# Kernel optimization log

Measured on AMD Instinct MI355X. Metric: run time of the kernel, lower is better.

The kernel has to match this reference:

```python
import jax, jax.numpy as jnp
import numpy as np

EPS = 1e-07
ROUTINGS = 3


def squash(s):
    # s: [..., d]
    n2 = jnp.sum(s * s, axis=-1, keepdims=True)
    return s * (n2 / (1.0 + n2) / jnp.sqrt(n2 + EPS))


def setup_inputs() -> dict:
    key = jax.random.key(0)
    k1, k2 = jax.random.split(key)
    B, I, P = 32, 2048, 16   # batch, input capsules, input capsule dim
    J, D = 32, 32            # output capsules, output capsule dim
    inputs = jax.random.normal(k1, (B, I, P), dtype=jnp.float32)
    # glorot-ish scale so squash operates in a reasonable range
    W = jax.random.normal(k2, (1, I, J, P, D), dtype=jnp.float32) * 0.05
    return {"inputs": inputs, "W": W}


def reference(inputs, W):
    # inputs: [B, I, P]; W: [1, I, J, P, D]
    Wm = W[0]  # [I, J, P, D]
    # u_hat[b,i,j,d] = sum_p W[i,j,p,d] * inputs[b,i,p]
    u_hat = jnp.einsum('bip,ijpd->bijd', inputs, Wm)  # [B, I, J, D]
    b = jnp.zeros(u_hat.shape[:3], dtype=u_hat.dtype)  # [B, I, J]
    v = None
    for it in range(ROUTINGS):
        c = jax.nn.softmax(b, axis=2)                    # over output capsules
        s = jnp.einsum('bij,bijd->bjd', c, u_hat)        # sum over input capsules
        v = squash(s)                                    # [B, J, D]
        if it < ROUTINGS - 1:
            b = b + jnp.einsum('bijd,bjd->bij', u_hat, v)  # agreement
    return v
```

## Files before the change

### kernel.cpp

```cpp
#include <hip/hip_runtime.h>

#define NB 32
#define NI 2048
#define NP 16
#define NJ 32
#define ND 32
#define EPSF 1e-7f

typedef __attribute__((ext_vector_type(8))) short bf16x8;
typedef __attribute__((ext_vector_type(16))) float f32x16;
typedef __attribute__((ext_vector_type(4))) float f32x4;

static __device__ __forceinline__ unsigned cvt_pk_bf16(float lo, float hi) {
  unsigned r;
  asm("v_cvt_pk_bf16_f32 %0, %1, %2" : "=v"(r) : "v"(lo), "v"(hi));
  return r;
}

static __device__ __forceinline__ f32x16 mfma_bf16(bf16x8 a, bf16x8 b, f32x16 c) {
  return __builtin_amdgcn_mfma_f32_32x32x16_bf16(a, b, c, 0, 0, 0);
}

static __device__ __forceinline__ float nt_load(const float* p) {
  return __builtin_nontemporal_load(p);
}

static __device__ __forceinline__ void lds_barrier() {
  asm volatile("s_waitcnt lgkmcnt(0)\n\ts_barrier" ::: "memory");
}

struct wraw { float f[8]; };
static __device__ __forceinline__ wraw load_wraw(const float* __restrict__ W,
                                                 int i, int j, int h, int d) {
  const float* wp = W + (((size_t)i * NJ + j) * NP + h * 8) * ND + d;
  wraw r;
#pragma unroll
  for (int e = 0; e < 8; ++e) r.f[e] = wp[e * ND];
  return r;
}
static __device__ __forceinline__ bf16x8 pack_wfrag(const wraw& r) {
  union { unsigned u[4]; bf16x8 v; } wf;
  wf.u[0] = cvt_pk_bf16(r.f[0], r.f[1]);
  wf.u[1] = cvt_pk_bf16(r.f[2], r.f[3]);
  wf.u[2] = cvt_pk_bf16(r.f[4], r.f[5]);
  wf.u[3] = cvt_pk_bf16(r.f[6], r.f[7]);
  return wf.v;
}

static __device__ __forceinline__ bf16x8 load_xfrag(const unsigned short* __restrict__ Xt,
                                                    int i, int b, int h) {
  return *(const bf16x8*)(Xt + ((size_t)i * NB + b) * NP + h * 8);
}

__global__ __launch_bounds__(256) void kern_prep(const float* __restrict__ in,
                                                 unsigned short* __restrict__ Xt) {
  const int t = blockIdx.x * 256 + threadIdx.x;
  const int rest = t >> 2;
  const int p4 = (t & 3) * 4;
  const int i = rest & (NI - 1);
  const int b = rest >> 11;
  f32x4 x = *(const f32x4*)(in + (size_t)rest * NP + p4);
  uint2 v;
  v.x = cvt_pk_bf16(x[0], x[1]);
  v.y = cvt_pk_bf16(x[2], x[3]);
  *(uint2*)(Xt + ((size_t)i * NB + b) * NP + p4) = v;
}

template <bool UNIFORM>
__global__ __attribute__((amdgpu_waves_per_eu(2, 2)))
__launch_bounds__(512) void kern_fused(const float* __restrict__ W,
                                       const unsigned short* __restrict__ Xt,
                                       const float* __restrict__ vsum,
                                       float* __restrict__ part,
                                       int ipb, int nch) {
  const int tid = threadIdx.x;
  const int w = tid >> 6;
  const int lane = tid & 63;
  const int b = lane & 31;
  const int h = lane >> 5;
  const int ch = blockIdx.x;
  const int i0 = ch * ipb;

  f32x4 vs[4][4];
  if (!UNIFORM) {
#pragma unroll
    for (int t = 0; t < 4; ++t) {
      const int j = w * 4 + t;
#pragma unroll
      for (int q = 0; q < 4; ++q)
        vs[t][q] = *(const f32x4*)(vsum + ((size_t)b * NJ + j) * ND + q * 8 + h * 4);
    }
  }

  f32x16 sacc[4] = {};
  __shared__ float lgt[NJ][33];

  wraw wr[4];
  bf16x8 xf;
#pragma unroll
  for (int t = 0; t < 4; ++t) wr[t] = load_wraw(W, i0, w * 4 + t, h, b);
  xf = load_xfrag(Xt, i0, b, h);

  for (int ii = 0; ii < ipb; ++ii) {
    const int i = i0 + ii;
    const int inext = (ii + 1 < ipb) ? i + 1 : i;
    wraw wrn[4];
#pragma unroll
    for (int t = 0; t < 4; ++t) wrn[t] = load_wraw(W, inext, w * 4 + t, h, b);
    const bf16x8 xfn = load_xfrag(Xt, inext, b, h);

    bf16x8 wf[4];
#pragma unroll
    for (int t = 0; t < 4; ++t) wf[t] = pack_wfrag(wr[t]);

    if (UNIFORM) {
#pragma unroll
      for (int t = 0; t < 4; ++t) sacc[t] = mfma_bf16(wf[t], xf, sacc[t]);
    } else {
      union { bf16x8 v; unsigned short s[8]; } xu; xu.v = xf;
      float xf32[8];
#pragma unroll
      for (int e = 0; e < 8; ++e)
        xf32[e] = __uint_as_float((unsigned)xu.s[e] << 16);

      float lg[4];
#pragma unroll
      for (int t = 0; t < 4; ++t) {
        f32x16 z = {};
        const f32x16 um = mfma_bf16(wf[t], xf, z);
        float p = 0.f;
#pragma unroll
        for (int r = 0; r < 16; ++r)
          p += um[r] * vs[t][r >> 2][r & 3];
        p += __shfl_xor(p, 32);
        lg[t] = p;
      }
      if (h == 0) {
#pragma unroll
        for (int t = 0; t < 4; ++t) lgt[w * 4 + t][b] = lg[t];
      }
      lds_barrier();
      float mx = -3.0e38f;
#pragma unroll
      for (int jj = 0; jj < NJ; ++jj) mx = fmaxf(mx, lgt[jj][b]);
      float den = 0.f;
#pragma unroll
      for (int jj = 0; jj < NJ; ++jj) den += expf(lgt[jj][b] - mx);
      const float inv = 1.0f / den;
#pragma unroll
      for (int t = 0; t < 4; ++t) {
        const float c = expf(lg[t] - mx) * inv;
        union { unsigned u[4]; bf16x8 v; } xc;
#pragma unroll
        for (int e = 0; e < 4; ++e)
          xc.u[e] = cvt_pk_bf16(xf32[2 * e] * c, xf32[2 * e + 1] * c);
        sacc[t] = mfma_bf16(wf[t], xc.v, sacc[t]);
      }
      lds_barrier();
    }

#pragma unroll
    for (int t = 0; t < 4; ++t) wr[t] = wrn[t];
    xf = xfn;
  }

#pragma unroll
  for (int t = 0; t < 4; ++t) {
    const int j = w * 4 + t;
    float* base = &part[(((size_t)j * nch + ch) * NB + b) * ND];
#pragma unroll
    for (int rq = 0; rq < 4; ++rq) {
      f32x4 v4;
#pragma unroll
      for (int e = 0; e < 4; ++e) {
        const float val = UNIFORM ? sacc[t][rq * 4 + e] * (1.0f / 32.0f)
                                  : sacc[t][rq * 4 + e];
        v4[e] = val;
      }
      *(f32x4*)(base + rq * 8 + 4 * h) = v4;
    }
  }
}

__global__ __launch_bounds__(1024) void kern_reduce1(const float* __restrict__ part,
                                                     float* __restrict__ part2,
                                                     int nch, int RG) {
  const int j = blockIdx.x / RG;
  const int r = blockIdx.x % RG;
  const int t = threadIdx.x;
  const int b = t >> 5;
  const int d = t & 31;
  float s = 0.f;
#pragma unroll 4
  for (int c = 0; c < 32; ++c)
    s += nt_load(&part[(((size_t)j * nch + r * 32 + c) * NB + b) * ND + d]);
  part2[(((size_t)j * RG + r) * NB + b) * ND + d] = s;
}

__global__ __launch_bounds__(1024) void kern_squash(const float* __restrict__ part2,
                                                    float* __restrict__ vsum,
                                                    float* __restrict__ out,
                                                    int mode, int RG) {
  const int j = blockIdx.x;
  const int t = threadIdx.x;
  const int b = t >> 5;
  const int d = t & 31;
  float s = 0.f;
  for (int r = 0; r < RG; ++r)
    s += nt_load(&part2[(((size_t)j * RG + r) * NB + b) * ND + d]);

  __shared__ float sl[32][33];
  __shared__ float fb[32];
  sl[b][d] = s;
  __syncthreads();
  if (t < 32) {
    float n2 = 0.f;
#pragma unroll
    for (int dd = 0; dd < ND; ++dd) { const float x = sl[t][dd]; n2 += x * x; }
    fb[t] = n2 / ((1.0f + n2) * sqrtf(n2 + EPSF));
  }
  __syncthreads();
  const float v = s * fb[b];
  const int idx = (b * NJ + j) * ND + d;
  if (mode == 0)      vsum[idx] = v;
  else if (mode == 1) vsum[idx] += v;
  else                out[idx] = v;
}

extern "C" void kernel_launch(void* const* d_in, const int* in_sizes, int n_in,
                              void* d_out, int out_size, void* d_ws, size_t ws_size,
                              hipStream_t stream) {
  const float* inp = (const float*)d_in[0];
  const float* W   = (const float*)d_in[1];
  if (n_in >= 2 && in_sizes[0] > in_sizes[1]) { const float* tmp = inp; inp = W; W = tmp; }
  float* out = (float*)d_out;
  char* ws = (char*)d_ws;
  (void)out_size;

  int nch = 256;
  while (nch > 32 &&
         (size_t)(2u << 20) + (size_t)nch * 131072u + 131072u +
             (size_t)(nch / 32) * 131072u > ws_size)
    nch >>= 1;
  const int ipb = NI / nch;
  const int RG = nch / 32;

  unsigned short* Xt = (unsigned short*)ws;
  float* part  = (float*)(ws + (2u << 20));
  float* vsum  = part + (size_t)NJ * nch * NB * ND;
  float* part2 = vsum + (size_t)NB * NJ * ND;

  kern_prep<<<1024, 256, 0, stream>>>(inp, Xt);

  kern_fused<true><<<nch, 512, 0, stream>>>(W, Xt, nullptr, part, ipb, nch);
  kern_reduce1<<<32 * RG, 1024, 0, stream>>>(part, part2, nch, RG);
  kern_squash<<<32, 1024, 0, stream>>>(part2, vsum, out, 0, RG);

  kern_fused<false><<<nch, 512, 0, stream>>>(W, Xt, vsum, part, ipb, nch);
  kern_reduce1<<<32 * RG, 1024, 0, stream>>>(part, part2, nch, RG);
  kern_squash<<<32, 1024, 0, stream>>>(part2, vsum, out, 1, RG);

  kern_fused<false><<<nch, 512, 0, stream>>>(W, Xt, vsum, part, ipb, nch);
  kern_reduce1<<<32 * RG, 1024, 0, stream>>>(part, part2, nch, RG);
  kern_squash<<<32, 1024, 0, stream>>>(part2, vsum, out, 2, RG);
}
```

Measured before the change: 153.0 us.

## Process two input capsules per iteration to halve barriers and vectorize softmax LDS

The fused routing kernel now handles two input capsules per loop iteration, so each pair shares one pair of LDS barriers instead of two pairs. Logits are stored transposed ([b][j]) so each lane reads its 32 logits with vector loads instead of scalar strided loads. The explicit software prefetch of the next capsule's W is dropped in favour of loading both capsules at the start of the iteration. This raises register pressure and assumes ipb is even; losing the prefetch may expose more global load latency.

```diff
diff --git a/kernel.cpp b/kernel.cpp
--- a/kernel.cpp
+++ b/kernel.cpp
@@ -93,75 +93,113 @@
   }
 
   f32x16 sacc[4] = {};
-  __shared__ float lgt[NJ][33];
-
-  wraw wr[4];
-  bf16x8 xf;
-#pragma unroll
-  for (int t = 0; t < 4; ++t) wr[t] = load_wraw(W, i0, w * 4 + t, h, b);
-  xf = load_xfrag(Xt, i0, b, h);
-
-  for (int ii = 0; ii < ipb; ++ii) {
-    const int i = i0 + ii;
-    const int inext = (ii + 1 < ipb) ? i + 1 : i;
-    wraw wrn[4];
-#pragma unroll
-    for (int t = 0; t < 4; ++t) wrn[t] = load_wraw(W, inext, w * 4 + t, h, b);
-    const bf16x8 xfn = load_xfrag(Xt, inext, b, h);
-
-    bf16x8 wf[4];
-#pragma unroll
-    for (int t = 0; t < 4; ++t) wf[t] = pack_wfrag(wr[t]);
+  __shared__ float lgtA[NB][33];
+  __shared__ float lgtB[NB][33];
+
+  for (int it = 0; it < ipb / 2; ++it) {
+    const int ia = i0 + 2 * it;
+    const int ib = ia + 1;
+
+    wraw wra[4], wrb[4];
+#pragma unroll
+    for (int t = 0; t < 4; ++t) wra[t] = load_wraw(W, ia, w * 4 + t, h, b);
+#pragma unroll
+    for (int t = 0; t < 4; ++t) wrb[t] = load_wraw(W, ib, w * 4 + t, h, b);
+    const bf16x8 xfa = load_xfrag(Xt, ia, b, h);
+    const bf16x8 xfb = load_xfrag(Xt, ib, b, h);
+
+    bf16x8 wfa[4], wfb[4];
+#pragma unroll
+    for (int t = 0; t < 4; ++t) wfa[t] = pack_wfrag(wra[t]);
+#pragma unroll
+    for (int t = 0; t < 4; ++t) wfb[t] = pack_wfrag(wrb[t]);
 
     if (UNIFORM) {
 #pragma unroll
-      for (int t = 0; t < 4; ++t) sacc[t] = mfma_bf16(wf[t], xf, sacc[t]);
+      for (int t = 0; t < 4; ++t) {
+        sacc[t] = mfma_bf16(wfa[t], xfa, sacc[t]);
+        sacc[t] = mfma_bf16(wfb[t], xfb, sacc[t]);
+      }
     } else {
-      union { bf16x8 v; unsigned short s[8]; } xu; xu.v = xf;
-      float xf32[8];
-#pragma unroll
-      for (int e = 0; e < 8; ++e)
-        xf32[e] = __uint_as_float((unsigned)xu.s[e] << 16);
-
-      float lg[4];
+      union { bf16x8 v; unsigned short s[8]; } xua, xub;
+      xua.v = xfa; xub.v = xfb;
+      float xfa32[8], xfb32[8];
+#pragma unroll
+      for (int e = 0; e < 8; ++e) {
+        xfa32[e] = __uint_as_float((unsigned)xua.s[e] << 16);
+        xfb32[e] = __uint_as_float((unsigned)xub.s[e] << 16);
+      }
+
+      union { float f[4]; f32x4 v; } lga, lgb;
 #pragma unroll
       for (int t = 0; t < 4; ++t) {
         f32x16 z = {};
-        const f32x16 um = mfma_bf16(wf[t], xf, z);
+        const f32x16 um = mfma_bf16(wfa[t], xfa, z);
         float p = 0.f;
 #pragma unroll
         for (int r = 0; r < 16; ++r)
           p += um[r] * vs[t][r >> 2][r & 3];
         p += __shfl_xor(p, 32);
-        lg[t] = p;
+        lga.f[t] = p;
+      }
+#pragma unroll
+      for (int t = 0; t < 4; ++t) {
+        f32x16 z = {};
+        const f32x16 um = mfma_bf16(wfb[t], xfb, z);
+        float p = 0.f;
+#pragma unroll
+        for (int r = 0; r < 16; ++r)
+          p += um[r] * vs[t][r >> 2][r & 3];
+        p += __shfl_xor(p, 32);
+        lgb.f[t] = p;
       }
       if (h == 0) {
-#pragma unroll
-        for (int t = 0; t < 4; ++t) lgt[w * 4 + t][b] = lg[t];
+        *(f32x4*)&lgtA[b][w * 4] = lga.v;
+        *(f32x4*)&lgtB[b][w * 4] = lgb.v;
       }
       lds_barrier();
-      float mx = -3.0e38f;
-#pragma unroll
-      for (int jj = 0; jj < NJ; ++jj) mx = fmaxf(mx, lgt[jj][b]);
-      float den = 0.f;
-#pragma unroll
-      for (int jj = 0; jj < NJ; ++jj) den += expf(lgt[jj][b] - mx);
-      const float inv = 1.0f / den;
-#pragma unroll
-      for (int t = 0; t < 4; ++t) {
-        const float c = expf(lg[t] - mx) * inv;
+
+      float mxa = -3.0e38f, mxb = -3.0e38f;
+      float va[8][4], vb[8][4];
+#pragma unroll
+      for (int q = 0; q < 8; ++q) {
+        const f32x4 ra = *(const f32x4*)&lgtA[b][q * 4];
+        const f32x4 rb = *(const f32x4*)&lgtB[b][q * 4];
+#pragma unroll
+        for (int e = 0; e < 4; ++e) {
+          va[q][e] = ra[e]; vb[q][e] = rb[e];
+          mxa = fmaxf(mxa, ra[e]); mxb = fmaxf(mxb, rb[e]);
+        }
+      }
+      float dena = 0.f, denb = 0.f;
+#pragma unroll
+      for (int q = 0; q < 8; ++q)
+#pragma unroll
+        for (int e = 0; e < 4; ++e) {
+          dena += expf(va[q][e] - mxa);
+          denb += expf(vb[q][e] - mxb);
+        }
+      const float inva = 1.0f / dena, invb = 1.0f / denb;
+#pragma unroll
+      for (int t = 0; t < 4; ++t) {
+        const float ca = expf(lga.f[t] - mxa) * inva;
         union { unsigned u[4]; bf16x8 v; } xc;
 #pragma unroll
         for (int e = 0; e < 4; ++e)
-          xc.u[e] = cvt_pk_bf16(xf32[2 * e] * c, xf32[2 * e + 1] * c);
-        sacc[t] = mfma_bf16(wf[t], xc.v, sacc[t]);
+          xc.u[e] = cvt_pk_bf16(xfa32[2 * e] * ca, xfa32[2 * e + 1] * ca);
+        sacc[t] = mfma_bf16(wfa[t], xc.v, sacc[t]);
+      }
+#pragma unroll
+      for (int t = 0; t < 4; ++t) {
+        const float cb = expf(lgb.f[t] - mxb) * invb;
+        union { unsigned u[4]; bf16x8 v; } xc;
+#pragma unroll
+        for (int e = 0; e < 4; ++e)
+          xc.u[e] = cvt_pk_bf16(xfb32[2 * e] * cb, xfb32[2 * e + 1] * cb);
+        sacc[t] = mfma_bf16(wfb[t], xc.v, sacc[t]);
       }
       lds_barrier();
     }
-
-#pragma unroll
-    for (int t = 0; t < 4; ++t) wr[t] = wrn[t];
-    xf = xfn;
   }
 
 #pragma unroll
```

Measured after the change: 175.4 us. 14.7% more time.
